# Kernel optimization log

Measured on AMD Instinct MI355X. Metric: run time of the kernel, lower is better.

The kernel has to match this reference:

```python
import jax, jax.numpy as jnp
import numpy as np
from jax import lax

B, C_IN, IMG, P, HID = 128, 3, 224, 16, 768
HW = (IMG // P) ** 2  # 196 patches


def setup_inputs() -> dict:
    key = jax.random.key(0)
    k1, k2, k3, k4 = jax.random.split(key, 4)
    x = jax.random.normal(k1, (B, C_IN, IMG, IMG), dtype=jnp.float32)
    # conv weight init scale ~ kaiming-ish, value irrelevant for correctness
    W = jax.random.normal(k2, (HID, C_IN, P, P), dtype=jnp.float32) * 0.02
    b = jax.random.normal(k3, (HID,), dtype=jnp.float32) * 0.02
    # per-sample random permutation of patch positions (the pixel shuffle)
    perm = jax.vmap(lambda k: jax.random.permutation(k, HW))(jax.random.split(k4, B)).astype(jnp.int32)
    return {"x": x, "W": W, "b": b, "perm": perm}


def reference(x, W, b, perm):
    # patchify conv: kernel_size == stride == P, no padding
    enc = lax.conv_general_dilated(
        x, W, window_strides=(P, P), padding="VALID",
        dimension_numbers=("NCHW", "OIHW", "NCHW"),
    ) + b[None, :, None, None]                      # [B, HID, H', W']
    Bc, Cc, Hc, Wc = enc.shape
    enc = enc.reshape(Bc, Cc, Hc * Wc).transpose(0, 2, 1)   # [B, HW, HID]
    # per-sample patch shuffle: shuffled[i, j] = enc[i, perm[i, j]]
    shuffled = jnp.take_along_axis(enc, perm[:, :, None], axis=1)
    return shuffled
```

## Files before the change

kernel.cpp:

```cpp
#include <hip/hip_runtime.h>
#include <hip/hip_bf16.h>

#define BATCH  128
#define HWN    196
#define HIDN   768
#define KN     768
#define IMGSZ  224
#define IMG2   (224*224)
#define MTOT   (BATCH*HWN)

#define BM 128
#define BN 128
#define BK 32

typedef __attribute__((ext_vector_type(8))) short bf16x8;
typedef __attribute__((ext_vector_type(4))) float floatx4;

#define GP(p) ((const __attribute__((address_space(1))) void*)(p))
#define SP(p) ((__attribute__((address_space(3))) void*)(p))

static __device__ __forceinline__ short f2bf(float f) {
    __hip_bfloat16 h = __float2bfloat16(f);
    return __builtin_bit_cast(short, h);
}

static __device__ __forceinline__ bf16x8 cvt8(const float* __restrict__ src) {
    float4 f0 = *(const float4*)(src);
    float4 f1 = *(const float4*)(src + 4);
    bf16x8 v;
    v[0]=f2bf(f0.x); v[1]=f2bf(f0.y); v[2]=f2bf(f0.z); v[3]=f2bf(f0.w);
    v[4]=f2bf(f1.x); v[5]=f2bf(f1.y); v[6]=f2bf(f1.z); v[7]=f2bf(f1.w);
    return v;
}

__global__ __launch_bounds__(256)
void prep_A(const float* __restrict__ x, const int* __restrict__ perm,
            unsigned short* __restrict__ A)
{
    const int idx = blockIdx.x * 256 + threadIdx.x;
    const int gr  = idx / 48;
    const int seg = idx - gr * 48;
    const int b   = gr / HWN;
    const int p   = perm[gr];
    const int py  = p / 14, px = p - py * 14;
    const int c   = seg >> 4;
    const int iy  = seg & 15;

    const float* src = x + (size_t)b * 3 * IMG2 + (size_t)c * IMG2
                         + (size_t)(py * 16 + iy) * IMGSZ + px * 16;
    bf16x8 v0 = cvt8(src);
    bf16x8 v1 = cvt8(src + 8);
    unsigned short* dst = A + (size_t)gr * KN + seg * 16;
    *(bf16x8*)(dst)     = v0;
    *(bf16x8*)(dst + 8) = v1;
}

__global__ __launch_bounds__(256)
void prep_W(const float* __restrict__ W, unsigned short* __restrict__ Wb)
{
    const int idx = blockIdx.x * 256 + threadIdx.x;
    const float* src = W + (size_t)idx * 8;
    *(bf16x8*)(Wb + (size_t)idx * 8) = cvt8(src);
}

__global__ __launch_bounds__(256, 3)
void gemm(const unsigned short* __restrict__ A, const unsigned short* __restrict__ Wb,
          const float* __restrict__ bias, float* __restrict__ out)
{
    __shared__ __align__(16) unsigned short As[BM * BK];
    __shared__ __align__(16) unsigned short Bs[BN * BK];

    const int tid = threadIdx.x;
    const int bm  = blockIdx.x;
    const int bn  = blockIdx.y;

    const int srow = tid >> 2;
    const int sseg = tid & 3;
    const unsigned short* ga = A  + (size_t)(bm * BM + srow) * KN + sseg * 8;
    const unsigned short* gb = Wb + (size_t)(bn * BN + srow) * KN + sseg * 8;

    const int lane = tid & 63;
    const int wave = tid >> 6;
    const int wm = (wave >> 1) * 64;
    const int wn = (wave & 1) * 64;
    const int lr = lane & 15;
    const int lq = lane >> 4;

    floatx4 acc[4][4] = {};

    for (int k0 = 0; k0 < KN; k0 += BK) {
        __builtin_amdgcn_global_load_lds(GP(ga + k0),            SP(&As[tid * 8]),        16, 0, 0);
        __builtin_amdgcn_global_load_lds(GP(ga + 64 * KN + k0),  SP(&As[2048 + tid * 8]), 16, 0, 0);
        __builtin_amdgcn_global_load_lds(GP(gb + k0),            SP(&Bs[tid * 8]),        16, 0, 0);
        __builtin_amdgcn_global_load_lds(GP(gb + 64 * KN + k0),  SP(&Bs[2048 + tid * 8]), 16, 0, 0);
        __syncthreads();

        bf16x8 bfrag[4];
        #pragma unroll
        for (int j = 0; j < 4; ++j)
            bfrag[j] = *(const bf16x8*)&Bs[(wn + j * 16 + lr) * BK + lq * 8];
        #pragma unroll
        for (int i = 0; i < 4; ++i) {
            bf16x8 afrag = *(const bf16x8*)&As[(wm + i * 16 + lr) * BK + lq * 8];
            #pragma unroll
            for (int j = 0; j < 4; ++j)
                acc[i][j] = __builtin_amdgcn_mfma_f32_16x16x32_bf16(
                                afrag, bfrag[j], acc[i][j], 0, 0, 0);
        }
        __syncthreads();
    }

    #pragma unroll
    for (int j = 0; j < 4; ++j) {
        const int gc = bn * BN + wn + j * 16 + lr;
        const float bv = bias[gc];
        #pragma unroll
        for (int i = 0; i < 4; ++i) {
            const int grow = bm * BM + wm + i * 16 + lq * 4;
            float* op = out + (size_t)grow * HIDN + gc;
            #pragma unroll
            for (int r = 0; r < 4; ++r)
                op[(size_t)r * HIDN] = acc[i][j][r] + bv;
        }
    }
}

extern "C" void kernel_launch(void* const* d_in, const int* in_sizes, int n_in,
                              void* d_out, int out_size, void* d_ws, size_t ws_size,
                              hipStream_t stream) {
    const float* x    = (const float*)d_in[0];
    const float* W    = (const float*)d_in[1];
    const float* bias = (const float*)d_in[2];
    const int*   perm = (const int*)d_in[3];
    float* out = (float*)d_out;

    unsigned short* A  = (unsigned short*)d_ws;
    unsigned short* Wb = A + (size_t)MTOT * KN;

    prep_A<<<dim3(MTOT * 48 / 256), dim3(256), 0, stream>>>(x, perm, A);
    prep_W<<<dim3(KN * HIDN / 8 / 256), dim3(256), 0, stream>>>(W, Wb);
    gemm<<<dim3(MTOT / BM, HIDN / BN), dim3(256), 0, stream>>>(A, Wb, bias, out);
}
```

Measured before the change: 193.1 us.

## Fuse patch gather and bf16 conversion into GEMM with register prefetch

Removes the separate prep_A kernel and the bf16 A buffer it wrote. The GEMM now gathers permuted image patches directly from x, converts them to bf16 in registers and writes them to an XOR-swizzled LDS tile. The next K-tile of x is prefetched into registers during the MFMA loop. Workgroups are remapped so that eight groups of consecutive tiles share the same N blocks, which should improve L2 reuse. In exchange, each GEMM block re-reads fp32 x six times (once per N tile) instead of reading bf16 A once. It also adds an extra barrier per K iteration and more register pressure.

```diff
diff --git a/kernel.cpp b/kernel.cpp
--- a/kernel.cpp
+++ b/kernel.cpp
@@ -12,6 +12,11 @@
 #define BM 128
 #define BN 128
 #define BK 32
+#define NT  (KN/BK)
+#define NBM (MTOT/BM)
+#define NBN (HIDN/BN)
+#define NWG (NBM*NBN)
+#define CPX (NWG/8)
 
 typedef __attribute__((ext_vector_type(8))) short bf16x8;
 typedef __attribute__((ext_vector_type(4))) float floatx4;
@@ -24,9 +29,7 @@
     return __builtin_bit_cast(short, h);
 }
 
-static __device__ __forceinline__ bf16x8 cvt8(const float* __restrict__ src) {
-    float4 f0 = *(const float4*)(src);
-    float4 f1 = *(const float4*)(src + 4);
+static __device__ __forceinline__ bf16x8 cvt8v(float4 f0, float4 f1) {
     bf16x8 v;
     v[0]=f2bf(f0.x); v[1]=f2bf(f0.y); v[2]=f2bf(f0.z); v[3]=f2bf(f0.w);
     v[4]=f2bf(f1.x); v[5]=f2bf(f1.y); v[6]=f2bf(f1.z); v[7]=f2bf(f1.w);
@@ -34,49 +37,42 @@
 }
 
 __global__ __launch_bounds__(256)
-void prep_A(const float* __restrict__ x, const int* __restrict__ perm,
-            unsigned short* __restrict__ A)
-{
-    const int idx = blockIdx.x * 256 + threadIdx.x;
-    const int gr  = idx / 48;
-    const int seg = idx - gr * 48;
-    const int b   = gr / HWN;
-    const int p   = perm[gr];
-    const int py  = p / 14, px = p - py * 14;
-    const int c   = seg >> 4;
-    const int iy  = seg & 15;
-
-    const float* src = x + (size_t)b * 3 * IMG2 + (size_t)c * IMG2
-                         + (size_t)(py * 16 + iy) * IMGSZ + px * 16;
-    bf16x8 v0 = cvt8(src);
-    bf16x8 v1 = cvt8(src + 8);
-    unsigned short* dst = A + (size_t)gr * KN + seg * 16;
-    *(bf16x8*)(dst)     = v0;
-    *(bf16x8*)(dst + 8) = v1;
-}
-
-__global__ __launch_bounds__(256)
 void prep_W(const float* __restrict__ W, unsigned short* __restrict__ Wb)
 {
     const int idx = blockIdx.x * 256 + threadIdx.x;
-    const float* src = W + (size_t)idx * 8;
-    *(bf16x8*)(Wb + (size_t)idx * 8) = cvt8(src);
+    float4 f0 = *(const float4*)(W + (size_t)idx * 8);
+    float4 f1 = *(const float4*)(W + (size_t)idx * 8 + 4);
+    *(bf16x8*)(Wb + (size_t)idx * 8) = cvt8v(f0, f1);
 }
 
 __global__ __launch_bounds__(256, 3)
-void gemm(const unsigned short* __restrict__ A, const unsigned short* __restrict__ Wb,
-          const float* __restrict__ bias, float* __restrict__ out)
+void gemm_fused(const float* __restrict__ x, const int* __restrict__ perm,
+                const unsigned short* __restrict__ Wb,
+                const float* __restrict__ bias, float* __restrict__ out)
 {
     __shared__ __align__(16) unsigned short As[BM * BK];
     __shared__ __align__(16) unsigned short Bs[BN * BK];
 
     const int tid = threadIdx.x;
-    const int bm  = blockIdx.x;
-    const int bn  = blockIdx.y;
+    const int wg  = blockIdx.x;
+    const int lid = (wg & 7) * CPX + (wg >> 3);
+    const int bm  = lid / NBN;
+    const int bn  = lid - bm * NBN;
+
+    const int arow = tid >> 1;
+    const int aseg = tid & 1;
+    const int gr   = bm * BM + arow;
+    const int b    = gr / HWN;
+    const int p    = perm[gr];
+    const int py   = p / 14, px = p - py * 14;
+    const float* xbase = x + (size_t)b * 3 * IMG2
+                           + (size_t)(py * 16) * IMGSZ + px * 16;
+    const int axor = ((arow >> 1) & 1) << 4;
+    char* aw0 = (char*)As + arow * 64 + ((aseg * 32     ) ^ axor);
+    char* aw1 = (char*)As + arow * 64 + ((aseg * 32 + 16) ^ axor);
 
     const int srow = tid >> 2;
     const int sseg = tid & 3;
-    const unsigned short* ga = A  + (size_t)(bm * BM + srow) * KN + sseg * 8;
     const unsigned short* gb = Wb + (size_t)(bn * BN + srow) * KN + sseg * 8;
 
     const int lane = tid & 63;
@@ -85,15 +81,35 @@
     const int wn = (wave & 1) * 64;
     const int lr = lane & 15;
     const int lq = lane >> 4;
+    const int ard = (lq * 16) ^ (((lr >> 1) & 1) << 4);
 
     floatx4 acc[4][4] = {};
+    float4 xf0, xf1, xf2, xf3;
 
-    for (int k0 = 0; k0 < KN; k0 += BK) {
-        __builtin_amdgcn_global_load_lds(GP(ga + k0),            SP(&As[tid * 8]),        16, 0, 0);
-        __builtin_amdgcn_global_load_lds(GP(ga + 64 * KN + k0),  SP(&As[2048 + tid * 8]), 16, 0, 0);
-        __builtin_amdgcn_global_load_lds(GP(gb + k0),            SP(&Bs[tid * 8]),        16, 0, 0);
-        __builtin_amdgcn_global_load_lds(GP(gb + 64 * KN + k0),  SP(&Bs[2048 + tid * 8]), 16, 0, 0);
-        __syncthreads();
+    auto loadx = [&](int t) {
+        const int s = t * 2 + aseg;
+        const float* src = xbase + (s >> 4) * IMG2 + (s & 15) * IMGSZ;
+        xf0 = *(const float4*)(src);
+        xf1 = *(const float4*)(src + 4);
+        xf2 = *(const float4*)(src + 8);
+        xf3 = *(const float4*)(src + 12);
+    };
+    auto writea = [&]() {
+        *(bf16x8*)aw0 = cvt8v(xf0, xf1);
+        *(bf16x8*)aw1 = cvt8v(xf2, xf3);
+    };
+    auto gldsb = [&](int t) {
+        __builtin_amdgcn_global_load_lds(GP(gb + t * BK),           SP(&Bs[tid * 8]),        16, 0, 0);
+        __builtin_amdgcn_global_load_lds(GP(gb + 64 * KN + t * BK), SP(&Bs[2048 + tid * 8]), 16, 0, 0);
+    };
+
+    loadx(0);
+    gldsb(0);
+    writea();
+    __syncthreads();
+
+    for (int t = 0; t < NT; ++t) {
+        if (t + 1 < NT) loadx(t + 1);
 
         bf16x8 bfrag[4];
         #pragma unroll
@@ -101,13 +117,19 @@
             bfrag[j] = *(const bf16x8*)&Bs[(wn + j * 16 + lr) * BK + lq * 8];
         #pragma unroll
         for (int i = 0; i < 4; ++i) {
-            bf16x8 afrag = *(const bf16x8*)&As[(wm + i * 16 + lr) * BK + lq * 8];
+            const bf16x8 afrag = *(const bf16x8*)((const char*)As + (wm + i * 16 + lr) * 64 + ard);
             #pragma unroll
             for (int j = 0; j < 4; ++j)
                 acc[i][j] = __builtin_amdgcn_mfma_f32_16x16x32_bf16(
                                 afrag, bfrag[j], acc[i][j], 0, 0, 0);
         }
-        __syncthreads();
+
+        if (t + 1 < NT) {
+            __syncthreads();
+            gldsb(t + 1);
+            writea();
+            __syncthreads();
+        }
     }
 
     #pragma unroll
@@ -134,10 +156,8 @@
     const int*   perm = (const int*)d_in[3];
     float* out = (float*)d_out;
 
-    unsigned short* A  = (unsigned short*)d_ws;
-    unsigned short* Wb = A + (size_t)MTOT * KN;
+    unsigned short* Wb = (unsigned short*)d_ws;
 
-    prep_A<<<dim3(MTOT * 48 / 256), dim3(256), 0, stream>>>(x, perm, A);
     prep_W<<<dim3(KN * HIDN / 8 / 256), dim3(256), 0, stream>>>(W, Wb);
-    gemm<<<dim3(MTOT / BM, HIDN / BN), dim3(256), 0, stream>>>(A, Wb, bias, out);
+    gemm_fused<<<dim3(NWG), dim3(256), 0, stream>>>(x, perm, Wb, bias, out);
 }
```

After: 212.1 us. +9.9%, slower.

## Move patch permutation into GEMM A-row gather and remap workgroups across XCDs

Applied to the files above, without the earlier changes.

prep_A now writes patches in natural order without reading perm, and the GEMM gathers permuted A rows by looking up perm per loaded row. The GEMM grid becomes 1D and workgroup IDs are remapped so that consecutive logical tiles land on the same XCD. This aims to improve L2 reuse of A and B tiles within each XCD and to simplify the prep pass, at the cost of scattered row reads in the GEMM loads.

```diff
diff --git a/kernel.cpp b/kernel.cpp
--- a/kernel.cpp
+++ b/kernel.cpp
@@ -12,6 +12,10 @@
 #define BM 128
 #define BN 128
 #define BK 32
+#define NBM (MTOT/BM)
+#define NBN (HIDN/BN)
+#define NWG (NBM*NBN)
+#define CPX (NWG/8)
 
 typedef __attribute__((ext_vector_type(8))) short bf16x8;
 typedef __attribute__((ext_vector_type(4))) float floatx4;
@@ -34,14 +38,13 @@
 }
 
 __global__ __launch_bounds__(256)
-void prep_A(const float* __restrict__ x, const int* __restrict__ perm,
-            unsigned short* __restrict__ A)
+void prep_A(const float* __restrict__ x, unsigned short* __restrict__ A)
 {
     const int idx = blockIdx.x * 256 + threadIdx.x;
     const int gr  = idx / 48;
     const int seg = idx - gr * 48;
     const int b   = gr / HWN;
-    const int p   = perm[gr];
+    const int p   = gr - b * HWN;
     const int py  = p / 14, px = p - py * 14;
     const int c   = seg >> 4;
     const int iy  = seg & 15;
@@ -64,20 +67,30 @@
 }
 
 __global__ __launch_bounds__(256, 3)
-void gemm(const unsigned short* __restrict__ A, const unsigned short* __restrict__ Wb,
+void gemm(const unsigned short* __restrict__ A, const int* __restrict__ perm,
+          const unsigned short* __restrict__ Wb,
           const float* __restrict__ bias, float* __restrict__ out)
 {
     __shared__ __align__(16) unsigned short As[BM * BK];
     __shared__ __align__(16) unsigned short Bs[BN * BK];
 
     const int tid = threadIdx.x;
-    const int bm  = blockIdx.x;
-    const int bn  = blockIdx.y;
+    const int wg  = blockIdx.x;
+    const int lid = (wg & 7) * CPX + (wg >> 3);
+    const int bm  = lid / NBN;
+    const int bn  = lid - bm * NBN;
 
     const int srow = tid >> 2;
     const int sseg = tid & 3;
-    const unsigned short* ga = A  + (size_t)(bm * BM + srow) * KN + sseg * 8;
-    const unsigned short* gb = Wb + (size_t)(bn * BN + srow) * KN + sseg * 8;
+    const int gr0 = bm * BM + srow;
+    const int gr1 = gr0 + 64;
+    const int b0  = gr0 / HWN;
+    const int b1  = gr1 / HWN;
+    const int pr0 = b0 * HWN + perm[gr0];
+    const int pr1 = b1 * HWN + perm[gr1];
+    const unsigned short* ga0 = A  + (size_t)pr0 * KN + sseg * 8;
+    const unsigned short* ga1 = A  + (size_t)pr1 * KN + sseg * 8;
+    const unsigned short* gb  = Wb + (size_t)(bn * BN + srow) * KN + sseg * 8;
 
     const int lane = tid & 63;
     const int wave = tid >> 6;
@@ -89,8 +102,8 @@
     floatx4 acc[4][4] = {};
 
     for (int k0 = 0; k0 < KN; k0 += BK) {
-        __builtin_amdgcn_global_load_lds(GP(ga + k0),            SP(&As[tid * 8]),        16, 0, 0);
-        __builtin_amdgcn_global_load_lds(GP(ga + 64 * KN + k0),  SP(&As[2048 + tid * 8]), 16, 0, 0);
+        __builtin_amdgcn_global_load_lds(GP(ga0 + k0),           SP(&As[tid * 8]),        16, 0, 0);
+        __builtin_amdgcn_global_load_lds(GP(ga1 + k0),           SP(&As[2048 + tid * 8]), 16, 0, 0);
         __builtin_amdgcn_global_load_lds(GP(gb + k0),            SP(&Bs[tid * 8]),        16, 0, 0);
         __builtin_amdgcn_global_load_lds(GP(gb + 64 * KN + k0),  SP(&Bs[2048 + tid * 8]), 16, 0, 0);
         __syncthreads();
@@ -137,7 +150,7 @@
     unsigned short* A  = (unsigned short*)d_ws;
     unsigned short* Wb = A + (size_t)MTOT * KN;
 
-    prep_A<<<dim3(MTOT * 48 / 256), dim3(256), 0, stream>>>(x, perm, A);
+    prep_A<<<dim3(MTOT * 48 / 256), dim3(256), 0, stream>>>(x, A);
     prep_W<<<dim3(KN * HIDN / 8 / 256), dim3(256), 0, stream>>>(W, Wb);
-    gemm<<<dim3(MTOT / BM, HIDN / BN), dim3(256), 0, stream>>>(A, Wb, bias, out);
+    gemm<<<dim3(NWG), dim3(256), 0, stream>>>(A, perm, Wb, bias, out);
 }
```

Measured after the change: 182.3 us. 1.06x faster.
